# Optimization experiments

Measured on AMD Instinct MI355X. Metric: run time of the kernel, lower is better.

## Reference

```python
import jax, jax.numpy as jnp
import numpy as np

NHEAD = 16
D_MODEL = 1024
DK = D_MODEL // NHEAD
Q_DIM = V_DIM = K_DIM = 1024
B, S = 2, 2048


def _xavier(key, shape):
    # xavier_uniform over last two dims (fan_in=shape[-2], fan_out=shape[-1])
    fan_in, fan_out = shape[-2], shape[-1]
    limit = float(np.sqrt(6.0 / (fan_in + fan_out)))
    return jax.random.uniform(key, shape, jnp.float32, -limit, limit)


def setup_inputs() -> dict:
    key = jax.random.key(0)
    kq, kv, kk, kwq, kwv, kwk = jax.random.split(key, 6)
    q = jax.random.normal(kq, (B, S, Q_DIM), jnp.float32)
    v = jax.random.normal(kv, (B, S, V_DIM), jnp.float32)
    k = jax.random.normal(kk, (B, S, K_DIM), jnp.float32)
    # causal mask: True = attend, matches masked_fill(~mask, -inf)
    causal = jnp.tril(jnp.ones((S, S), dtype=bool))
    attn_mask = jnp.broadcast_to(causal, (B, S, S))
    q_proj_mats = _xavier(kwq, (NHEAD, Q_DIM, DK))
    v_proj_mats = _xavier(kwv, (NHEAD, V_DIM, DK))
    k_proj_mats = _xavier(kwk, (NHEAD, K_DIM, DK))
    return {"q": q, "v": v, "k": k, "attn_mask": attn_mask,
            "q_proj_mats": q_proj_mats, "v_proj_mats": v_proj_mats,
            "k_proj_mats": k_proj_mats}


def reference(q, v, k, attn_mask, q_proj_mats, v_proj_mats, k_proj_mats):
    bsz, seq_len, _ = q.shape
    # per-head projections: [B,S,dim] x [H,dim,dk] -> [B,H,S,dk]
    qp = jnp.einsum('bsk,hkd->bhsd', q, q_proj_mats)
    vp = jnp.einsum('bsk,hkd->bhsd', v, v_proj_mats)
    kp = jnp.einsum('bsk,hkd->bhsd', k, k_proj_mats)
    # NOTE: original scales by sqrt(d_model), not sqrt(dk)
    scale = 1.0 / jnp.sqrt(jnp.float32(D_MODEL))
    logits = jnp.einsum('bhqd,bhkd->bhqk', qp, kp) * scale  # [B,H,S,S]
    logits = jnp.where(attn_mask[:, None, :, :], logits, -jnp.inf)
    score = jax.nn.softmax(logits, axis=-1)
    weighted = jnp.einsum('bhkd,bhqk->bqhd', vp, score)  # [B,S,H,dk]
    return weighted.reshape(bsz, seq_len, -1)
```

## Files before the change

kernel.cpp:

```cpp
#include <hip/hip_runtime.h>
#include <cstdint>
#include <cstddef>

#define NB 2
#define NS 2048
#define NH 16
#define NDK 64
#define NDM 1024
#define SCALE 0.03125f

using u16 = unsigned short;
typedef __attribute__((ext_vector_type(8))) short bf16x8;
typedef __attribute__((ext_vector_type(4))) float f32x4;

#define AS1 __attribute__((address_space(1)))
#define AS3 __attribute__((address_space(3)))

__device__ __forceinline__ u16 f2bf(float f) {
    unsigned int x = __float_as_uint(f);
    return (u16)((x + 0x7FFFu + ((x >> 16) & 1u)) >> 16);
}
__device__ __forceinline__ unsigned int packbf(float f0, float f1) {
    return __builtin_amdgcn_perm(__float_as_uint(f1), __float_as_uint(f0),
                                 0x07060302u);
}

__global__ __launch_bounds__(256)
void prep(const float* __restrict__ q, const float* __restrict__ v,
          const float* __restrict__ kkk,
          const float* __restrict__ qw, const float* __restrict__ vw,
          const float* __restrict__ kw,
          u16* __restrict__ xt, u16* __restrict__ wbt, int nxblk)
{
    __shared__ __align__(16) u16 SH[64 * 72];
    const int t = threadIdx.x;
    const int bid = blockIdx.x;
    if (bid < nxblk) {
        int z   = bid >> 7;
        int rem = bid & 127;
        int mt  = rem >> 2;
        int kq  = rem & 3;
        const float* X = (z == 0) ? q : (z == 1) ? v : kkk;
        const float* src = X + (size_t)mt * 128 * NDM;
        u16* dst = xt + (((size_t)z * 32 + mt) << 17);
        const int row = t >> 3;
        const int cl  = (t & 7) * 4;
        const int pl  = (t & 7) >> 1;
        const int hf  = (t & 1) * 4;
        for (int kk = kq * 8; kk < kq * 8 + 8; ++kk) {
            #pragma unroll
            for (int i = 0; i < 4; ++i) {
                int ml = row + 32 * i;
                float4 f = *reinterpret_cast<const float4*>(
                    src + (size_t)ml * NDM + kk * 32 + cl);
                uint2 u;
                u.x = packbf(f.x, f.y);
                u.y = packbf(f.z, f.w);
                *reinterpret_cast<uint2*>(&SH[(pl * 128 + ml) * 8 + hf]) = u;
            }
            __syncthreads();
            {
                uint4 o0 = *reinterpret_cast<uint4*>(&SH[(2 * t) * 8]);
                uint4 o1 = *reinterpret_cast<uint4*>(&SH[(2 * t + 1) * 8]);
                u16* dd = dst + ((size_t)kk << 12) + 2 * t * 8;
                *reinterpret_cast<uint4*>(dd)     = o0;
                *reinterpret_cast<uint4*>(dd + 8) = o1;
            }
            __syncthreads();
        }
    } else {
        int b  = bid - nxblk;
        int z  = b >> 8;
        int h  = (b >> 4) & 15;
        int k0 = (b & 15) * 64;
        const float* W = ((z == 0) ? qw : (z == 1) ? vw : kw)
                         + (size_t)h * NDM * NDK;
        {
            int kr = t >> 2, d0 = (t & 3) * 16;
            const float* src = W + (size_t)(k0 + kr) * NDK + d0;
            #pragma unroll
            for (int c = 0; c < 4; ++c) {
                float4 f = *reinterpret_cast<const float4*>(src + c * 4);
                SH[(d0 + c * 4 + 0) * 72 + kr] = f2bf(f.x);
                SH[(d0 + c * 4 + 1) * 72 + kr] = f2bf(f.y);
                SH[(d0 + c * 4 + 2) * 72 + kr] = f2bf(f.z);
                SH[(d0 + c * 4 + 3) * 72 + kr] = f2bf(f.w);
            }
        }
        __syncthreads();
        {
            int pl = t >> 6, d = t & 63;
            int nt = h >> 1;
            int cb = pl * 128 + (h & 1) * 64 + d;
            #pragma unroll
            for (int ki = 0; ki < 2; ++ki) {
                uint4 val = *reinterpret_cast<const uint4*>(
                    &SH[d * 72 + ki * 32 + pl * 8]);
                size_t base = (((size_t)z * 8 + nt) * 32 + (k0 >> 5) + ki) << 12;
                *reinterpret_cast<uint4*>(wbt + base + cb * 8) = val;
            }
        }
    }
}

__device__ __forceinline__ void gemm_epilogue(
    f32x4 acc[4][4], int z, int m0, int n0, int wm, int wn,
    int quad, int l15, u16* __restrict__ O)
{
    const int bb = m0 >> 11;
    const int hh = (n0 + wn) >> 6;
    const size_t headT = ((size_t)(bb * NH + hh)) << 17;
    if (z == 2) {
        #pragma unroll
        for (int mi = 0; mi < 4; ++mi) {
            #pragma unroll
            for (int r = 0; r < 4; ++r) {
                int s = (m0 + wm + mi * 16 + quad * 4 + r) & 2047;
                size_t tb = headT + ((size_t)(s >> 6) << 12) + (s & 63) * 8 + (l15 & 7);
                int chb = l15 >> 3;
                #pragma unroll
                for (int ni = 0; ni < 4; ++ni)
                    O[tb + (ni * 2 + chb) * 512] = f2bf(acc[mi][ni][r]);
            }
        }
    } else if (z == 1) {
        #pragma unroll
        for (int mi = 0; mi < 4; ++mi) {
            #pragma unroll
            for (int r = 0; r < 4; ++r) {
                int s = (m0 + wm + mi * 16 + quad * 4 + r) & 2047;
                size_t tb = headT + ((size_t)(s >> 6) << 12)
                          + ((s & 63) >> 3) * 512 + (s & 7);
                #pragma unroll
                for (int ni = 0; ni < 4; ++ni)
                    O[tb + (ni * 16 + l15) * 8] = f2bf(acc[mi][ni][r]);
            }
        }
    } else {
        #pragma unroll
        for (int mi = 0; mi < 4; ++mi) {
            #pragma unroll
            for (int r = 0; r < 4; ++r) {
                int s = (m0 + wm + mi * 16 + quad * 4 + r) & 2047;
                size_t rb = ((size_t)(bb * NH + hh) * NS + s) * NDK;
                #pragma unroll
                for (int ni = 0; ni < 4; ++ni)
                    O[rb + ni * 16 + l15] = f2bf(acc[mi][ni][r]);
            }
        }
    }
}

__global__ __launch_bounds__(256)
void gemm_xt(const u16* __restrict__ xt, const u16* __restrict__ wbt,
             u16* __restrict__ qp, u16* __restrict__ vp,
             u16* __restrict__ kp)
{
    __shared__ __align__(16) u16 SA[2][4096];
    __shared__ __align__(16) u16 SB[2][4096];

    const int t    = threadIdx.x;
    const int lane = t & 63;
    const int w    = t >> 6;
    const int quad = lane >> 4, l15 = lane & 15;
    const int mt = blockIdx.x, nt = blockIdx.y, z = blockIdx.z;

    const u16* As = xt + (((size_t)z * 32 + mt) << 17);
    const u16* Bs = wbt + (((size_t)z * 8 + nt) << 17);
    u16* O = (z == 0) ? qp : (z == 1) ? vp : kp;
    const int wm = (w & 1) * 64, wn = (w >> 1) * 64;

    #pragma unroll
    for (int i = 0; i < 2; ++i) {
        int c = i * 256 + t;
        __builtin_amdgcn_global_load_lds((const AS1 void*)(As + c * 8),
                                         (AS3 void*)&SA[0][c * 8], 16, 0, 0);
        __builtin_amdgcn_global_load_lds((const AS1 void*)(Bs + c * 8),
                                         (AS3 void*)&SB[0][c * 8], 16, 0, 0);
    }

    f32x4 acc[4][4] = {};

    #pragma unroll 2
    for (int kk = 0; kk < 32; ++kk) {
        const int cur = kk & 1;
        __syncthreads();
        if (kk < 31) {
            const size_t off = (size_t)(kk + 1) << 12;
            #pragma unroll
            for (int i = 0; i < 2; ++i) {
                int c = i * 256 + t;
                __builtin_amdgcn_global_load_lds(
                    (const AS1 void*)(As + off + c * 8),
                    (AS3 void*)&SA[cur ^ 1][c * 8], 16, 0, 0);
                __builtin_amdgcn_global_load_lds(
                    (const AS1 void*)(Bs + off + c * 8),
                    (AS3 void*)&SB[cur ^ 1][c * 8], 16, 0, 0);
            }
        }
        bf16x8 af[4], bfr[4];
        #pragma unroll
        for (int mi = 0; mi < 4; ++mi)
            af[mi] = *reinterpret_cast<const bf16x8*>(
                &SA[cur][quad * 1024 + (wm + mi * 16 + l15) * 8]);
        #pragma unroll
        for (int ni = 0; ni < 4; ++ni)
            bfr[ni] = *reinterpret_cast<const bf16x8*>(
                &SB[cur][quad * 1024 + (wn + ni * 16 + l15) * 8]);
        #pragma unroll
        for (int mi = 0; mi < 4; ++mi)
            #pragma unroll
            for (int ni = 0; ni < 4; ++ni)
                acc[mi][ni] = __builtin_amdgcn_mfma_f32_16x16x32_bf16(
                    af[mi], bfr[ni], acc[mi][ni], 0, 0, 0);
    }

    gemm_epilogue(acc, z, mt * 128, nt * 128, wm, wn, quad, l15, O);
}

__global__ __launch_bounds__(256)
void gemm_pack(const float* __restrict__ q, const float* __restrict__ v,
               const float* __restrict__ kkk, const u16* __restrict__ wbt,
               u16* __restrict__ qp, u16* __restrict__ vp,
               u16* __restrict__ kp)
{
    __shared__ __align__(16) u16 SA[2][4096];
    __shared__ __align__(16) u16 SB[2][4096];

    const int t    = threadIdx.x;
    const int lane = t & 63;
    const int w    = t >> 6;
    const int quad = lane >> 4, l15 = lane & 15;
    const int m0 = blockIdx.x * 128;
    const int n0 = blockIdx.y * 128;
    const int z  = blockIdx.z;

    const float* X = (z == 0) ? q : (z == 1) ? v : kkk;
    const u16* Wb2 = wbt + (((size_t)z * 8 + (n0 >> 7)) << 17);
    u16* O = (z == 0) ? qp : (z == 1) ? vp : kp;

    const int wm = (w & 1) * 64, wn = (w >> 1) * 64;
    const int arow = t >> 3;
    const int acol = (t & 7) * 4;
    const int apl  = (t & 7) >> 1;
    const int aj   = (t & 1) * 4;
    const float* xa = X + (size_t)(m0 + arow) * NDM + acol;

    float4 fA[4];
    #pragma unroll
    for (int i = 0; i < 4; ++i)
        fA[i] = *reinterpret_cast<const float4*>(xa + (size_t)(32 * i) * NDM);
    #pragma unroll
    for (int i = 0; i < 2; ++i) {
        int c = i * 256 + t;
        __builtin_amdgcn_global_load_lds((const AS1 void*)(Wb2 + c * 8),
                                         (AS3 void*)&SB[0][c * 8], 16, 0, 0);
    }

    f32x4 acc[4][4] = {};

    #pragma unroll 2
    for (int kk = 0; kk < 32; ++kk) {
        const int cur = kk & 1;
        #pragma unroll
        for (int i = 0; i < 4; ++i) {
            uint2 u;
            u.x = packbf(fA[i].x, fA[i].y);
            u.y = packbf(fA[i].z, fA[i].w);
            *reinterpret_cast<uint2*>(
                &SA[cur][apl * 1024 + (arow + 32 * i) * 8 + aj]) = u;
        }
        __syncthreads();

        if (kk < 31) {
            const int kn = (kk + 1) * 32;
            const float* p = xa + kn;
            #pragma unroll
            for (int i = 0; i < 4; ++i)
                fA[i] = *reinterpret_cast<const float4*>(p + (size_t)(32 * i) * NDM);
            const u16* src = Wb2 + ((size_t)(kk + 1) << 12);
            #pragma unroll
            for (int i = 0; i < 2; ++i) {
                int c = i * 256 + t;
                __builtin_amdgcn_global_load_lds((const AS1 void*)(src + c * 8),
                                                 (AS3 void*)&SB[cur ^ 1][c * 8], 16, 0, 0);
            }
        }

        bf16x8 af[4], bfr[4];
        #pragma unroll
        for (int mi = 0; mi < 4; ++mi)
            af[mi] = *reinterpret_cast<const bf16x8*>(
                &SA[cur][quad * 1024 + (wm + mi * 16 + l15) * 8]);
        #pragma unroll
        for (int ni = 0; ni < 4; ++ni)
            bfr[ni] = *reinterpret_cast<const bf16x8*>(
                &SB[cur][quad * 1024 + (wn + ni * 16 + l15) * 8]);
        #pragma unroll
        for (int mi = 0; mi < 4; ++mi)
            #pragma unroll
            for (int ni = 0; ni < 4; ++ni)
                acc[mi][ni] = __builtin_amdgcn_mfma_f32_16x16x32_bf16(
                    af[mi], bfr[ni], acc[mi][ni], 0, 0, 0);
    }

    gemm_epilogue(acc, z, m0, n0, wm, wn, quad, l15, O);
}

__global__ __launch_bounds__(256)
void attn_kernel(const u16* __restrict__ QP, const u16* __restrict__ KP,
                 const u16* __restrict__ VT, float* __restrict__ Out)
{
    __shared__ __align__(16) u16 KB[2][4096];
    __shared__ __align__(16) u16 VB[2][4096];
    __shared__ __align__(16) u16 Pl[4][1024];

    const int t    = threadIdx.x;
    const int w    = t >> 6;
    const int lane = t & 63;
    const int quad = lane >> 4, l15 = lane & 15;

    const int qt = 31 - (blockIdx.x >> 5);
    const int bh = blockIdx.x & 31;
    const size_t headQ = (size_t)bh * NS * NDK;
    const size_t headT = (size_t)bh << 17;
    const int q0 = qt * 64 + w * 16;

    bf16x8 qf0, qf1;
    {
        const u16* qa = QP + headQ + (size_t)(q0 + l15) * NDK + quad * 8;
        qf0 = *reinterpret_cast<const bf16x8*>(qa);
        qf1 = *reinterpret_cast<const bf16x8*>(qa + 32);
    }

    f32x4 o[4] = {};
    float lsum = 0.0f;

    const int swz = (l15 & 3) << 4;

    #pragma unroll
    for (int i = 0; i < 2; ++i) {
        int c = i * 256 + t;
        __builtin_amdgcn_global_load_lds((const AS1 void*)(KP + headT + c * 8),
                                         (AS3 void*)&KB[0][c * 8], 16, 0, 0);
        __builtin_amdgcn_global_load_lds((const AS1 void*)(VT + headT + c * 8),
                                         (AS3 void*)&VB[0][c * 8], 16, 0, 0);
    }

    for (int kt = 0; kt <= qt; ++kt) {
        const int cur = kt & 1;
        __syncthreads();
        if (kt < qt) {
            const int nb = cur ^ 1;
            const size_t tb = headT + ((size_t)(kt + 1) << 12);
            #pragma unroll
            for (int i = 0; i < 2; ++i) {
                int c = i * 256 + t;
                __builtin_amdgcn_global_load_lds((const AS1 void*)(KP + tb + c * 8),
                                                 (AS3 void*)&KB[nb][c * 8], 16, 0, 0);
                __builtin_amdgcn_global_load_lds((const AS1 void*)(VT + tb + c * 8),
                                                 (AS3 void*)&VB[nb][c * 8], 16, 0, 0);
            }
        }

        f32x4 s[4];
        #pragma unroll
        for (int g = 0; g < 4; ++g) {
            const int rowoff = (g * 16 + l15) * 8;
            bf16x8 k0 = *reinterpret_cast<const bf16x8*>(&KB[cur][quad * 512 + rowoff]);
            bf16x8 k1 = *reinterpret_cast<const bf16x8*>(&KB[cur][(quad + 4) * 512 + rowoff]);
            f32x4 z = {};
            s[g] = __builtin_amdgcn_mfma_f32_16x16x32_bf16(k1, qf1,
                     __builtin_amdgcn_mfma_f32_16x16x32_bf16(k0, qf0, z, 0, 0, 0),
                     0, 0, 0);
        }

        const bool diag = (kt == qt);
        #pragma unroll
        for (int g = 0; g < 4; ++g) {
            float p0 = __expf(s[g][0] * SCALE);
            float p1 = __expf(s[g][1] * SCALE);
            float p2 = __expf(s[g][2] * SCALE);
            float p3 = __expf(s[g][3] * SCALE);
            if (diag) {
                const int kb = g * 16 + quad * 4;
                const int qr = w * 16 + l15;
                if (kb + 0 > qr) p0 = 0.0f;
                if (kb + 1 > qr) p1 = 0.0f;
                if (kb + 2 > qr) p2 = 0.0f;
                if (kb + 3 > qr) p3 = 0.0f;
            }
            lsum += (p0 + p1) + (p2 + p3);
            uint2 u;
            u.x = packbf(p0, p1);
            u.y = packbf(p2, p3);
            *reinterpret_cast<uint2*>(
                &Pl[w][l15 * 64 + ((g * 16 + quad * 4) ^ swz)]) = u;
        }
        asm volatile("" ::: "memory");

        bf16x8 pa0 = *reinterpret_cast<const bf16x8*>(
            &Pl[w][l15 * 64 + ((quad * 8) ^ swz)]);
        bf16x8 pa1 = *reinterpret_cast<const bf16x8*>(
            &Pl[w][l15 * 64 + ((32 + quad * 8) ^ swz)]);
        #pragma unroll
        for (int d = 0; d < 4; ++d) {
            const int rowoff = (d * 16 + l15) * 8;
            bf16x8 v0 = *reinterpret_cast<const bf16x8*>(&VB[cur][quad * 512 + rowoff]);
            bf16x8 v1 = *reinterpret_cast<const bf16x8*>(&VB[cur][(quad + 4) * 512 + rowoff]);
            o[d] = __builtin_amdgcn_mfma_f32_16x16x32_bf16(pa1, v1,
                     __builtin_amdgcn_mfma_f32_16x16x32_bf16(pa0, v0, o[d], 0, 0, 0),
                     0, 0, 0);
        }
    }

    lsum += __shfl_xor(lsum, 16, 64);
    lsum += __shfl_xor(lsum, 32, 64);

    const int bb = bh >> 4, h = bh & 15;
    #pragma unroll
    for (int r = 0; r < 4; ++r) {
        float inv = 1.0f / __shfl(lsum, quad * 4 + r, 64);
        size_t ob = ((size_t)bb * NS + q0 + quad * 4 + r) * NDM + h * 64 + l15;
        #pragma unroll
        for (int d = 0; d < 4; ++d)
            Out[ob + d * 16] = o[d][r] * inv;
    }
}

extern "C" void kernel_launch(void* const* d_in, const int* in_sizes, int n_in,
                              void* d_out, int out_size, void* d_ws, size_t ws_size,
                              hipStream_t stream) {
    const float* q  = (const float*)d_in[0];
    const float* v  = (const float*)d_in[1];
    const float* k  = (const float*)d_in[2];
    const float* qw = (const float*)d_in[4];
    const float* vw = (const float*)d_in[5];
    const float* kw = (const float*)d_in[6];

    const size_t PSZ = (size_t)NB * NH * NS * NDK;
    u16* wbt = (u16*)d_ws;
    u16* qp  = wbt + (size_t)3 * NDM * NDM;
    u16* vp  = qp + PSZ;
    u16* kp  = vp + PSZ;
    u16* xt  = kp + PSZ;

    const size_t NEED_XT = ((size_t)3 * NDM * NDM + 3 * PSZ
                            + (size_t)3 * 4096 * NDM) * 2;
    const bool xtpath = (ws_size >= NEED_XT);
    const int nx = xtpath ? 384 : 0;

    prep<<<dim3(768 + nx), dim3(256), 0, stream>>>(
        q, v, k, qw, vw, kw, xtpath ? xt : (u16*)d_ws, wbt, nx);

    if (xtpath)
        gemm_xt<<<dim3(32, 8, 3), dim3(256), 0, stream>>>(xt, wbt, qp, vp, kp);
    else
        gemm_pack<<<dim3(32, 8, 3), dim3(256), 0, stream>>>(q, v, k, wbt,
                                                            qp, vp, kp);

    attn_kernel<<<dim3(32 * 32), dim3(256), 0, stream>>>(qp, kp, vp,
                                                         (float*)d_out);
}
```

Measured before the change: 197.4 us.

## Pair complementary causal query tiles per block to balance work and share K/V loads

Each attention block now handles two query tiles, qt and 31-qt, for the same head. Both tiles share each K/V tile staged in LDS, so every block does equal causal work and the grid is halved to 512 blocks. The K and V fragments are hoisted into registers once per iteration and reused for both tiles, and the P swizzle is widened from 4 to 8 row phases. In exchange the kernel uses more registers and has half as many blocks, which may reduce occupancy and the latency hiding across waves.

New measurement: 200.4 us. No clear change (+1.5%).

```diff
diff --git a/kernel.cpp b/kernel.cpp
--- a/kernel.cpp
+++ b/kernel.cpp
@@ -320,23 +320,28 @@
     const int lane = t & 63;
     const int quad = lane >> 4, l15 = lane & 15;
 
-    const int qt = 31 - (blockIdx.x >> 5);
+    const int pi = blockIdx.x >> 5;
     const int bh = blockIdx.x & 31;
+    const int qtA = 31 - pi;
+    const int qtB = pi;
     const size_t headQ = (size_t)bh * NS * NDK;
     const size_t headT = (size_t)bh << 17;
-    const int q0 = qt * 64 + w * 16;
-
-    bf16x8 qf0, qf1;
+    const int q0A = qtA * 64 + w * 16, q0B = qtB * 64 + w * 16;
+
+    bf16x8 qfA0, qfA1, qfB0, qfB1;
     {
-        const u16* qa = QP + headQ + (size_t)(q0 + l15) * NDK + quad * 8;
-        qf0 = *reinterpret_cast<const bf16x8*>(qa);
-        qf1 = *reinterpret_cast<const bf16x8*>(qa + 32);
-    }
-
-    f32x4 o[4] = {};
-    float lsum = 0.0f;
-
-    const int swz = (l15 & 3) << 4;
+        const u16* qa = QP + headQ + (size_t)(q0A + l15) * NDK + quad * 8;
+        qfA0 = *reinterpret_cast<const bf16x8*>(qa);
+        qfA1 = *reinterpret_cast<const bf16x8*>(qa + 32);
+        const u16* qb = QP + headQ + (size_t)(q0B + l15) * NDK + quad * 8;
+        qfB0 = *reinterpret_cast<const bf16x8*>(qb);
+        qfB1 = *reinterpret_cast<const bf16x8*>(qb + 32);
+    }
+
+    f32x4 oA[4] = {}, oB[4] = {};
+    float lsA = 0.0f, lsB = 0.0f;
+
+    const int sw8 = (l15 & 7) << 3;
 
     #pragma unroll
     for (int i = 0; i < 2; ++i) {
@@ -347,10 +352,10 @@
                                          (AS3 void*)&VB[0][c * 8], 16, 0, 0);
     }
 
-    for (int kt = 0; kt <= qt; ++kt) {
+    for (int kt = 0; kt <= qtA; ++kt) {
         const int cur = kt & 1;
         __syncthreads();
-        if (kt < qt) {
+        if (kt < qtA) {
             const int nb = cur ^ 1;
             const size_t tb = headT + ((size_t)(kt + 1) << 12);
             #pragma unroll
@@ -363,26 +368,39 @@
             }
         }
 
-        f32x4 s[4];
+        bf16x8 k0[4], k1[4], v0[4], v1[4];
         #pragma unroll
         for (int g = 0; g < 4; ++g) {
-            const int rowoff = (g * 16 + l15) * 8;
-            bf16x8 k0 = *reinterpret_cast<const bf16x8*>(&KB[cur][quad * 512 + rowoff]);
-            bf16x8 k1 = *reinterpret_cast<const bf16x8*>(&KB[cur][(quad + 4) * 512 + rowoff]);
+            const int ro = (g * 16 + l15) * 8;
+            k0[g] = *reinterpret_cast<const bf16x8*>(&KB[cur][quad * 512 + ro]);
+            k1[g] = *reinterpret_cast<const bf16x8*>(&KB[cur][(quad + 4) * 512 + ro]);
+            v0[g] = *reinterpret_cast<const bf16x8*>(&VB[cur][quad * 512 + ro]);
+            v1[g] = *reinterpret_cast<const bf16x8*>(&VB[cur][(quad + 4) * 512 + ro]);
+        }
+
+        const bool doB = (kt <= qtB);
+        const bool dA = (kt == qtA), dB = (kt == qtB);
+
+        f32x4 sA[4], sB[4];
+        #pragma unroll
+        for (int g = 0; g < 4; ++g) {
             f32x4 z = {};
-            s[g] = __builtin_amdgcn_mfma_f32_16x16x32_bf16(k1, qf1,
-                     __builtin_amdgcn_mfma_f32_16x16x32_bf16(k0, qf0, z, 0, 0, 0),
-                     0, 0, 0);
-        }
-
-        const bool diag = (kt == qt);
+            sA[g] = __builtin_amdgcn_mfma_f32_16x16x32_bf16(k1[g], qfA1,
+                      __builtin_amdgcn_mfma_f32_16x16x32_bf16(k0[g], qfA0, z, 0, 0, 0),
+                      0, 0, 0);
+            if (doB)
+                sB[g] = __builtin_amdgcn_mfma_f32_16x16x32_bf16(k1[g], qfB1,
+                          __builtin_amdgcn_mfma_f32_16x16x32_bf16(k0[g], qfB0, z, 0, 0, 0),
+                          0, 0, 0);
+        }
+
         #pragma unroll
         for (int g = 0; g < 4; ++g) {
-            float p0 = __expf(s[g][0] * SCALE);
-            float p1 = __expf(s[g][1] * SCALE);
-            float p2 = __expf(s[g][2] * SCALE);
-            float p3 = __expf(s[g][3] * SCALE);
-            if (diag) {
+            float p0 = __expf(sA[g][0] * SCALE);
+            float p1 = __expf(sA[g][1] * SCALE);
+            float p2 = __expf(sA[g][2] * SCALE);
+            float p3 = __expf(sA[g][3] * SCALE);
+            if (dA) {
                 const int kb = g * 16 + quad * 4;
                 const int qr = w * 16 + l15;
                 if (kb + 0 > qr) p0 = 0.0f;
@@ -390,41 +408,78 @@
                 if (kb + 2 > qr) p2 = 0.0f;
                 if (kb + 3 > qr) p3 = 0.0f;
             }
-            lsum += (p0 + p1) + (p2 + p3);
+            lsA += (p0 + p1) + (p2 + p3);
             uint2 u;
             u.x = packbf(p0, p1);
             u.y = packbf(p2, p3);
             *reinterpret_cast<uint2*>(
-                &Pl[w][l15 * 64 + ((g * 16 + quad * 4) ^ swz)]) = u;
+                &Pl[w][l15 * 64 + ((g * 16 + quad * 4) ^ sw8)]) = u;
         }
         asm volatile("" ::: "memory");
-
-        bf16x8 pa0 = *reinterpret_cast<const bf16x8*>(
-            &Pl[w][l15 * 64 + ((quad * 8) ^ swz)]);
-        bf16x8 pa1 = *reinterpret_cast<const bf16x8*>(
-            &Pl[w][l15 * 64 + ((32 + quad * 8) ^ swz)]);
-        #pragma unroll
-        for (int d = 0; d < 4; ++d) {
-            const int rowoff = (d * 16 + l15) * 8;
-            bf16x8 v0 = *reinterpret_cast<const bf16x8*>(&VB[cur][quad * 512 + rowoff]);
-            bf16x8 v1 = *reinterpret_cast<const bf16x8*>(&VB[cur][(quad + 4) * 512 + rowoff]);
-            o[d] = __builtin_amdgcn_mfma_f32_16x16x32_bf16(pa1, v1,
-                     __builtin_amdgcn_mfma_f32_16x16x32_bf16(pa0, v0, o[d], 0, 0, 0),
-                     0, 0, 0);
-        }
-    }
-
-    lsum += __shfl_xor(lsum, 16, 64);
-    lsum += __shfl_xor(lsum, 32, 64);
+        bf16x8 paA0 = *reinterpret_cast<const bf16x8*>(
+            &Pl[w][l15 * 64 + ((quad * 8) ^ sw8)]);
+        bf16x8 paA1 = *reinterpret_cast<const bf16x8*>(
+            &Pl[w][l15 * 64 + ((32 + quad * 8) ^ sw8)]);
+        asm volatile("" ::: "memory");
+        #pragma unroll
+        for (int d = 0; d < 4; ++d)
+            oA[d] = __builtin_amdgcn_mfma_f32_16x16x32_bf16(paA1, v1[d],
+                      __builtin_amdgcn_mfma_f32_16x16x32_bf16(paA0, v0[d], oA[d], 0, 0, 0),
+                      0, 0, 0);
+
+        if (doB) {
+            #pragma unroll
+            for (int g = 0; g < 4; ++g) {
+                float p0 = __expf(sB[g][0] * SCALE);
+                float p1 = __expf(sB[g][1] * SCALE);
+                float p2 = __expf(sB[g][2] * SCALE);
+                float p3 = __expf(sB[g][3] * SCALE);
+                if (dB) {
+                    const int kb = g * 16 + quad * 4;
+                    const int qr = w * 16 + l15;
+                    if (kb + 0 > qr) p0 = 0.0f;
+                    if (kb + 1 > qr) p1 = 0.0f;
+                    if (kb + 2 > qr) p2 = 0.0f;
+                    if (kb + 3 > qr) p3 = 0.0f;
+                }
+                lsB += (p0 + p1) + (p2 + p3);
+                uint2 u;
+                u.x = packbf(p0, p1);
+                u.y = packbf(p2, p3);
+                *reinterpret_cast<uint2*>(
+                    &Pl[w][l15 * 64 + ((g * 16 + quad * 4) ^ sw8)]) = u;
+            }
+            asm volatile("" ::: "memory");
+            bf16x8 paB0 = *reinterpret_cast<const bf16x8*>(
+                &Pl[w][l15 * 64 + ((quad * 8) ^ sw8)]);
+            bf16x8 paB1 = *reinterpret_cast<const bf16x8*>(
+                &Pl[w][l15 * 64 + ((32 + quad * 8) ^ sw8)]);
+            asm volatile("" ::: "memory");
+            #pragma unroll
+            for (int d = 0; d < 4; ++d)
+                oB[d] = __builtin_amdgcn_mfma_f32_16x16x32_bf16(paB1, v1[d],
+                          __builtin_amdgcn_mfma_f32_16x16x32_bf16(paB0, v0[d], oB[d], 0, 0, 0),
+                          0, 0, 0);
+        }
+    }
+
+    lsA += __shfl_xor(lsA, 16, 64);
+    lsA += __shfl_xor(lsA, 32, 64);
+    lsB += __shfl_xor(lsB, 16, 64);
+    lsB += __shfl_xor(lsB, 32, 64);
 
     const int bb = bh >> 4, h = bh & 15;
     #pragma unroll
     for (int r = 0; r < 4; ++r) {
-        float inv = 1.0f / __shfl(lsum, quad * 4 + r, 64);
-        size_t ob = ((size_t)bb * NS + q0 + quad * 4 + r) * NDM + h * 64 + l15;
-        #pragma unroll
-        for (int d = 0; d < 4; ++d)
-            Out[ob + d * 16] = o[d][r] * inv;
+        float ia = 1.0f / __shfl(lsA, quad * 4 + r, 64);
+        float ib = 1.0f / __shfl(lsB, quad * 4 + r, 64);
+        size_t oa = ((size_t)bb * NS + q0A + quad * 4 + r) * NDM + h * 64 + l15;
+        size_t ob = ((size_t)bb * NS + q0B + quad * 4 + r) * NDM + h * 64 + l15;
+        #pragma unroll
+        for (int d = 0; d < 4; ++d) {
+            Out[oa + d * 16] = oA[d][r] * ia;
+            Out[ob + d * 16] = oB[d][r] * ib;
+        }
     }
 }
 
@@ -459,6 +514,6 @@
         gemm_pack<<<dim3(32, 8, 3), dim3(256), 0, stream>>>(q, v, k, wbt,
                                                             qp, vp, kp);
 
-    attn_kernel<<<dim3(32 * 32), dim3(256), 0, stream>>>(qp, kp, vp,
-                                                         (float*)d_out);
-}
+    attn_kernel<<<dim3(512), dim3(256), 0, stream>>>(qp, kp, vp,
+                                                     (float*)d_out);
+}
```

## Split attention work across key columns per wave and keep P in registers

Applied to the files above, without the earlier changes.

Each wave now owns a 16-key slice of the key tile and computes scores for all 64 query rows, so P feeds the PV MFMA (16x16x16) straight from registers instead of making a round trip through LDS. The softmax scale and log2e are folded into the Q projection epilogue so exp2 can be used directly. Partial outputs and row sums are reduced across the four waves through shared memory at the end. Launch bounds request 3 blocks per SU. The trade-off is more accumulator registers and an extra cross-wave reduction epilogue.

Result: slower. 206.9 us (+4.8%).

```diff
diff --git a/kernel.cpp b/kernel.cpp
--- a/kernel.cpp
+++ b/kernel.cpp
@@ -8,9 +8,11 @@
 #define NDK 64
 #define NDM 1024
 #define SCALE 0.03125f
+#define QSCALE 0.045084220f
 
 using u16 = unsigned short;
 typedef __attribute__((ext_vector_type(8))) short bf16x8;
+typedef __attribute__((ext_vector_type(4))) short bf16x4;
 typedef __attribute__((ext_vector_type(4))) float f32x4;
 
 #define AS1 __attribute__((address_space(1)))
@@ -23,6 +25,26 @@
 __device__ __forceinline__ unsigned int packbf(float f0, float f1) {
     return __builtin_amdgcn_perm(__float_as_uint(f1), __float_as_uint(f0),
                                  0x07060302u);
+}
+__device__ __forceinline__ float fexp2(float x) {
+#if defined(__HIP_DEVICE_COMPILE__) && __has_builtin(__builtin_amdgcn_exp2f)
+    return __builtin_amdgcn_exp2f(x);
+#else
+    return __builtin_exp2f(x);
+#endif
+}
+__device__ __forceinline__ f32x4 mfma16(bf16x4 a, bf16x4 b, f32x4 c) {
+#if !defined(__HIP_DEVICE_COMPILE__)
+    (void)a; (void)b;
+    return c;
+#elif __has_builtin(__builtin_amdgcn_mfma_f32_16x16x16bf16_1k)
+    return __builtin_amdgcn_mfma_f32_16x16x16bf16_1k(a, b, c, 0, 0, 0);
+#else
+    typedef __attribute__((ext_vector_type(4))) __bf16 bf16v4;
+    return __builtin_amdgcn_mfma_f32_16x16x16_bf16(
+        *reinterpret_cast<bf16v4*>(&a), *reinterpret_cast<bf16v4*>(&b),
+        c, 0, 0, 0);
+#endif
 }
 
 __global__ __launch_bounds__(256)
@@ -145,7 +167,7 @@
                 size_t rb = ((size_t)(bb * NH + hh) * NS + s) * NDK;
                 #pragma unroll
                 for (int ni = 0; ni < 4; ++ni)
-                    O[rb + ni * 16 + l15] = f2bf(acc[mi][ni][r]);
+                    O[rb + ni * 16 + l15] = f2bf(acc[mi][ni][r] * QSCALE);
             }
         }
     }
@@ -307,13 +329,15 @@
     gemm_epilogue(acc, z, m0, n0, wm, wn, quad, l15, O);
 }
 
-__global__ __launch_bounds__(256)
+__global__ __launch_bounds__(256, 3)
 void attn_kernel(const u16* __restrict__ QP, const u16* __restrict__ KP,
                  const u16* __restrict__ VT, float* __restrict__ Out)
 {
-    __shared__ __align__(16) u16 KB[2][4096];
-    __shared__ __align__(16) u16 VB[2][4096];
-    __shared__ __align__(16) u16 Pl[4][1024];
+    __shared__ __align__(16) u16 SMEM[16384];
+    __shared__ float LS[4][4][16];
+
+    u16* KB = SMEM;
+    u16* VB = SMEM + 8192;
 
     const int t    = threadIdx.x;
     const int w    = t >> 6;
@@ -324,107 +348,152 @@
     const int bh = blockIdx.x & 31;
     const size_t headQ = (size_t)bh * NS * NDK;
     const size_t headT = (size_t)bh << 17;
-    const int q0 = qt * 64 + w * 16;
-
-    bf16x8 qf0, qf1;
-    {
-        const u16* qa = QP + headQ + (size_t)(q0 + l15) * NDK + quad * 8;
-        qf0 = *reinterpret_cast<const bf16x8*>(qa);
-        qf1 = *reinterpret_cast<const bf16x8*>(qa + 32);
-    }
-
-    f32x4 o[4] = {};
-    float lsum = 0.0f;
-
-    const int swz = (l15 & 3) << 4;
+    const int q0 = qt * 64;
+
+    bf16x8 qf[4][2];
+    #pragma unroll
+    for (int qg = 0; qg < 4; ++qg) {
+        const u16* qa = QP + headQ + (size_t)(q0 + qg * 16 + l15) * NDK + quad * 8;
+        qf[qg][0] = *reinterpret_cast<const bf16x8*>(qa);
+        qf[qg][1] = *reinterpret_cast<const bf16x8*>(qa + 32);
+    }
+
+    f32x4 o[4][4] = {};
+    float ls[4] = {};
 
     #pragma unroll
     for (int i = 0; i < 2; ++i) {
         int c = i * 256 + t;
         __builtin_amdgcn_global_load_lds((const AS1 void*)(KP + headT + c * 8),
-                                         (AS3 void*)&KB[0][c * 8], 16, 0, 0);
+                                         (AS3 void*)&KB[c * 8], 16, 0, 0);
         __builtin_amdgcn_global_load_lds((const AS1 void*)(VT + headT + c * 8),
-                                         (AS3 void*)&VB[0][c * 8], 16, 0, 0);
+                                         (AS3 void*)&VB[c * 8], 16, 0, 0);
     }
 
     for (int kt = 0; kt <= qt; ++kt) {
         const int cur = kt & 1;
         __syncthreads();
         if (kt < qt) {
+            const size_t tb = headT + ((size_t)(kt + 1) << 12);
             const int nb = cur ^ 1;
-            const size_t tb = headT + ((size_t)(kt + 1) << 12);
             #pragma unroll
             for (int i = 0; i < 2; ++i) {
                 int c = i * 256 + t;
                 __builtin_amdgcn_global_load_lds((const AS1 void*)(KP + tb + c * 8),
-                                                 (AS3 void*)&KB[nb][c * 8], 16, 0, 0);
+                                                 (AS3 void*)&KB[nb * 4096 + c * 8], 16, 0, 0);
                 __builtin_amdgcn_global_load_lds((const AS1 void*)(VT + tb + c * 8),
-                                                 (AS3 void*)&VB[nb][c * 8], 16, 0, 0);
-            }
-        }
-
-        f32x4 s[4];
-        #pragma unroll
-        for (int g = 0; g < 4; ++g) {
-            const int rowoff = (g * 16 + l15) * 8;
-            bf16x8 k0 = *reinterpret_cast<const bf16x8*>(&KB[cur][quad * 512 + rowoff]);
-            bf16x8 k1 = *reinterpret_cast<const bf16x8*>(&KB[cur][(quad + 4) * 512 + rowoff]);
+                                                 (AS3 void*)&VB[nb * 4096 + c * 8], 16, 0, 0);
+            }
+        }
+        const u16* KBc = KB + cur * 4096;
+        const u16* VBc = VB + cur * 4096;
+
+        bf16x8 k0 = *reinterpret_cast<const bf16x8*>(
+            &KBc[quad * 512 + (w * 16 + l15) * 8]);
+        bf16x8 k1 = *reinterpret_cast<const bf16x8*>(
+            &KBc[(quad + 4) * 512 + (w * 16 + l15) * 8]);
+
+        const bool diag = (kt == qt);
+        bf16x4 pf[4];
+        #pragma unroll
+        for (int qg = 0; qg < 4; ++qg) {
             f32x4 z = {};
-            s[g] = __builtin_amdgcn_mfma_f32_16x16x32_bf16(k1, qf1,
-                     __builtin_amdgcn_mfma_f32_16x16x32_bf16(k0, qf0, z, 0, 0, 0),
-                     0, 0, 0);
-        }
-
-        const bool diag = (kt == qt);
-        #pragma unroll
-        for (int g = 0; g < 4; ++g) {
-            float p0 = __expf(s[g][0] * SCALE);
-            float p1 = __expf(s[g][1] * SCALE);
-            float p2 = __expf(s[g][2] * SCALE);
-            float p3 = __expf(s[g][3] * SCALE);
+            f32x4 s = __builtin_amdgcn_mfma_f32_16x16x32_bf16(k1, qf[qg][1],
+                        __builtin_amdgcn_mfma_f32_16x16x32_bf16(k0, qf[qg][0], z, 0, 0, 0),
+                        0, 0, 0);
+            float p0 = fexp2(s[0]);
+            float p1 = fexp2(s[1]);
+            float p2 = fexp2(s[2]);
+            float p3 = fexp2(s[3]);
             if (diag) {
-                const int kb = g * 16 + quad * 4;
-                const int qr = w * 16 + l15;
+                const int kb = w * 16 + quad * 4;
+                const int qr = qg * 16 + l15;
                 if (kb + 0 > qr) p0 = 0.0f;
                 if (kb + 1 > qr) p1 = 0.0f;
                 if (kb + 2 > qr) p2 = 0.0f;
                 if (kb + 3 > qr) p3 = 0.0f;
             }
-            lsum += (p0 + p1) + (p2 + p3);
-            uint2 u;
-            u.x = packbf(p0, p1);
-            u.y = packbf(p2, p3);
-            *reinterpret_cast<uint2*>(
-                &Pl[w][l15 * 64 + ((g * 16 + quad * 4) ^ swz)]) = u;
-        }
-        asm volatile("" ::: "memory");
-
-        bf16x8 pa0 = *reinterpret_cast<const bf16x8*>(
-            &Pl[w][l15 * 64 + ((quad * 8) ^ swz)]);
-        bf16x8 pa1 = *reinterpret_cast<const bf16x8*>(
-            &Pl[w][l15 * 64 + ((32 + quad * 8) ^ swz)]);
+            ls[qg] += (p0 + p1) + (p2 + p3);
+            union { unsigned int u[2]; bf16x4 v; } pu;
+            pu.u[0] = packbf(p0, p1);
+            pu.u[1] = packbf(p2, p3);
+            pf[qg] = pu.v;
+        }
+
         #pragma unroll
         for (int d = 0; d < 4; ++d) {
-            const int rowoff = (d * 16 + l15) * 8;
-            bf16x8 v0 = *reinterpret_cast<const bf16x8*>(&VB[cur][quad * 512 + rowoff]);
-            bf16x8 v1 = *reinterpret_cast<const bf16x8*>(&VB[cur][(quad + 4) * 512 + rowoff]);
-            o[d] = __builtin_amdgcn_mfma_f32_16x16x32_bf16(pa1, v1,
-                     __builtin_amdgcn_mfma_f32_16x16x32_bf16(pa0, v0, o[d], 0, 0, 0),
-                     0, 0, 0);
-        }
-    }
-
-    lsum += __shfl_xor(lsum, 16, 64);
-    lsum += __shfl_xor(lsum, 32, 64);
-
+            const bf16x4 vf = *reinterpret_cast<const bf16x4*>(
+                &VBc[(2 * w + (quad >> 1)) * 512 + (d * 16 + l15) * 8 + (quad & 1) * 4]);
+            #pragma unroll
+            for (int qg = 0; qg < 4; ++qg)
+                o[qg][d] = mfma16(pf[qg], vf, o[qg][d]);
+        }
+    }
+
+    #pragma unroll
+    for (int qg = 0; qg < 4; ++qg) {
+        ls[qg] += __shfl_xor(ls[qg], 16, 64);
+        ls[qg] += __shfl_xor(ls[qg], 32, 64);
+    }
+
+    __syncthreads();
+    if (quad == 0) {
+        #pragma unroll
+        for (int qg = 0; qg < 4; ++qg) LS[w][qg][l15] = ls[qg];
+    }
+    __syncthreads();
+    float inv[4];
+    #pragma unroll
+    for (int qg = 0; qg < 4; ++qg)
+        inv[qg] = 1.0f / (LS[0][qg][l15] + LS[1][qg][l15]
+                        + LS[2][qg][l15] + LS[3][qg][l15]);
+
+    float* SC = reinterpret_cast<float*>(SMEM);
     const int bb = bh >> 4, h = bh & 15;
     #pragma unroll
-    for (int r = 0; r < 4; ++r) {
-        float inv = 1.0f / __shfl(lsum, quad * 4 + r, 64);
-        size_t ob = ((size_t)bb * NS + q0 + quad * 4 + r) * NDM + h * 64 + l15;
-        #pragma unroll
-        for (int d = 0; d < 4; ++d)
-            Out[ob + d * 16] = o[d][r] * inv;
+    for (int round = 0; round < 2; ++round) {
+        const int qgA = round * 2, qgB = round * 2 + 1;
+        if (w != qgA) {
+            #pragma unroll
+            for (int d = 0; d < 4; ++d)
+                *reinterpret_cast<f32x4*>(
+                    SC + ((qgA & 1) * 4 + w) * 1024 + (d * 16 + l15) * 16 + quad * 4)
+                    = o[qgA][d];
+        }
+        if (w != qgB) {
+            #pragma unroll
+            for (int d = 0; d < 4; ++d)
+                *reinterpret_cast<f32x4*>(
+                    SC + ((qgB & 1) * 4 + w) * 1024 + (d * 16 + l15) * 16 + quad * 4)
+                    = o[qgB][d];
+        }
+        __syncthreads();
+        if (w == qgA || w == qgB) {
+            const int qg = w;
+            const float invq = (w == qgA) ? inv[qgA] : inv[qgB];
+            f32x4 acc[4];
+            #pragma unroll
+            for (int d = 0; d < 4; ++d) {
+                acc[d] = (w == qgA) ? o[qgA][d] : o[qgB][d];
+                #pragma unroll
+                for (int w2 = 0; w2 < 4; ++w2) {
+                    if (w2 != qg)
+                        acc[d] += *reinterpret_cast<const f32x4*>(
+                            SC + ((qg & 1) * 4 + w2) * 1024
+                               + (d * 16 + l15) * 16 + quad * 4);
+                }
+            }
+            #pragma unroll
+            for (int r = 0; r < 4; ++r) {
+                const float iv = __shfl(invq, quad * 4 + r, 64);
+                const size_t ob = ((size_t)bb * NS + q0 + qg * 16 + quad * 4 + r)
+                                  * NDM + h * 64 + l15;
+                #pragma unroll
+                for (int d = 0; d < 4; ++d)
+                    Out[ob + d * 16] = acc[d][r] * iv;
+            }
+        }
+        if (round == 0) __syncthreads();
     }
 }
 
```
